# Performance work log

Measured on AMD Instinct MI355X. Metric: run time of the kernel, lower is better.

Reference implementation:

```python
import jax, jax.numpy as jnp
import numpy as np

EMB = 1024
HID = 2048
HEADS = 16
CONV = 4


def causal_conv1d(z, w):
    # z: [B, H, T], w: [H, K] depthwise causal conv
    K = w.shape[1]
    T = z.shape[-1]
    zp = jnp.pad(z, ((0, 0), (0, 0), (K - 1, 0)))  # [B, H, T+K-1]
    out = jnp.zeros_like(z)
    for k in range(K):  # tiny fixed loop over taps (K<=4)
        out = out + w[None, :, k, None] * jax.lax.dynamic_slice_in_dim(zp, k, T, axis=2)
    return out


def linear_scan(a, b):
    # h_t = a_t * h_{t-1} + b_t along last axis; associative scan
    def combine(c1, c2):
        a1, b1 = c1
        a2, b2 = c2
        return a1 * a2, a2 * b1 + b2
    _, h = jax.lax.associative_scan(combine, (a, b), axis=-1)
    return h


def setup_inputs() -> dict:
    key = jax.random.key(0)
    k1, k2, k3, k4 = jax.random.split(key, 4)
    x = jax.random.normal(k1, (4, 2048, EMB), dtype=jnp.float32)
    w1 = jax.random.normal(k2, (3 * HID, EMB), dtype=jnp.float32) * (EMB ** -0.5)
    w2 = jax.random.normal(k3, (EMB, HID), dtype=jnp.float32) * (HID ** -0.5)
    conv_weight = jax.random.normal(k4, (HID, CONV), dtype=jnp.float32) * (CONV ** -0.5)
    return {"x": x, "w1": w1, "w2": w2, "conv_weight": conv_weight}


def reference(x, w1, w2, conv_weight):
    bsz, seq_len, _ = x.shape
    head_dim = HID // HEADS
    y = jnp.einsum("bse,he->bsh", x, w1)  # [B, S, 3*HID]
    out1, z, h = jnp.split(y, 3, axis=-1)
    z = jnp.swapaxes(z, 1, 2)  # [B, HID, S]
    h = jnp.swapaxes(h, 1, 2)
    z = causal_conv1d(z, conv_weight)
    z = jax.nn.sigmoid(z)
    z = z.reshape(bsz * HEADS, head_dim, seq_len)
    h = h.reshape(bsz * HEADS, head_dim, seq_len)
    h = linear_scan(1.0 - z, z * h)
    out2 = jnp.swapaxes(h.reshape(bsz, HID, seq_len), 1, 2)  # [B, S, HID]
    out = jax.nn.silu(out1) * out2
    return jnp.einsum("bsh,eh->bse", out, w2)
```

## Files before the change

### kernel.cpp

```cpp
#include <hip/hip_runtime.h>
#include <cstdint>

#define EMB 1024
#define HID 2048
#define BATCH 4
#define SEQ 2048
#define MROWS (BATCH * SEQ)
#define N1 (3 * HID)
#define K1 EMB
#define N2 EMB
#define K2 HID

#define NX (MROWS * EMB)
#define NW1 (N1 * K1)
#define NW2 (N2 * K2)

#define SEG 32
#define SLEN (SEQ / SEG)

typedef unsigned short ushort_t;
typedef __bf16 bf16x8 __attribute__((ext_vector_type(8)));
typedef float f32x4 __attribute__((ext_vector_type(4)));
typedef ushort_t us4 __attribute__((ext_vector_type(4)));

__device__ __forceinline__ ushort_t f2bf(float f) {
    uint32_t u = __builtin_bit_cast(uint32_t, f);
    u += 0x7fffu + ((u >> 16) & 1u);
    return (ushort_t)(u >> 16);
}
__device__ __forceinline__ float bf2f(ushort_t h) {
    uint32_t u = ((uint32_t)h) << 16;
    return __builtin_bit_cast(float, u);
}
__device__ __forceinline__ float bflo(uint32_t v) {
    return __builtin_bit_cast(float, v << 16);
}
__device__ __forceinline__ float bfhi(uint32_t v) {
    return __builtin_bit_cast(float, v & 0xffff0000u);
}
__device__ __forceinline__ float sigm(float x) {
    return 1.f / (1.f + __expf(-x));
}

__device__ __forceinline__ void gload_lds16(const ushort_t* g, const ushort_t* l) {
    __builtin_amdgcn_global_load_lds(
        (const __attribute__((address_space(1))) void*)(uintptr_t)(g),
        (__attribute__((address_space(3))) void*)(uint32_t)(uintptr_t)(l),
        16, 0, 0);
}

__global__ __launch_bounds__(256) void cvt_kernel(
    const float* __restrict__ x, const float* __restrict__ w1,
    const float* __restrict__ w2, ushort_t* __restrict__ xb,
    ushort_t* __restrict__ w1b, ushort_t* __restrict__ w2b) {
    const int i = (blockIdx.x * 256 + threadIdx.x) * 4;
    const float* s;
    ushort_t* d;
    if (i < NX) {
        s = x + i; d = xb + i;
    } else if (i < NX + NW1) {
        s = w1 + (i - NX); d = w1b + (i - NX);
    } else {
        s = w2 + (i - NX - NW1); d = w2b + (i - NX - NW1);
    }
    const float4 v = *(const float4*)s;
    us4 o;
    o.x = f2bf(v.x); o.y = f2bf(v.y); o.z = f2bf(v.z); o.w = f2bf(v.w);
    *(us4*)d = o;
}

template <bool OUT_BF16>
__global__ __launch_bounds__(256) void gemm_bt(
    const ushort_t* __restrict__ A, const ushort_t* __restrict__ B,
    void* __restrict__ Cv, int M, int N, int K) {
    __shared__ ushort_t sA[2 * 128 * 32];
    __shared__ ushort_t sB[2 * 128 * 32];

    const int tid  = threadIdx.x;
    const int lane = tid & 63;
    const int wave = tid >> 6;
    const int quad = lane >> 4;
    const int l16  = lane & 15;
    const long tm0 = (long)blockIdx.y * 128;
    const long tn0 = (long)blockIdx.x * 128;
    const int wm = (wave & 1) * 64;
    const int wn = (wave >> 1) * 64;

    f32x4 acc[4][4] = {};

    const int ar0 = tid >> 2;
    const int ar1 = (tid + 256) >> 2;
    const int kq  = (tid & 3) ^ ((ar0 >> 1) & 3);
    const int ac  = kq * 8;
    const ushort_t* gA = A + (size_t)tm0 * K;
    const ushort_t* gB = B + (size_t)tn0 * K;

    const int rsw = (l16 >> 1) & 3;
    const int aoff = (quad ^ rsw) * 8 + l16 * 32;

    for (int k0 = 0; k0 < K; k0 += 64) {
        __syncthreads();
#pragma unroll
        for (int p = 0; p < 2; ++p) {
            const int kp = k0 + p * 32;
            ushort_t* pA = &sA[p * 4096];
            ushort_t* pB = &sB[p * 4096];
            gload_lds16(gA + (size_t)ar0 * K + kp + ac, pA + wave * 512);
            gload_lds16(gA + (size_t)ar1 * K + kp + ac, pA + 2048 + wave * 512);
            gload_lds16(gB + (size_t)ar0 * K + kp + ac, pB + wave * 512);
            gload_lds16(gB + (size_t)ar1 * K + kp + ac, pB + 2048 + wave * 512);
        }
        __syncthreads();

#pragma unroll
        for (int p = 0; p < 2; ++p) {
            const ushort_t* pA = &sA[p * 4096];
            const ushort_t* pB = &sB[p * 4096];
            bf16x8 af[4], bfr[4];
#pragma unroll
            for (int i = 0; i < 4; ++i)
                af[i] = *(const bf16x8*)&pA[(wm + i * 16) * 32 + aoff];
#pragma unroll
            for (int j = 0; j < 4; ++j)
                bfr[j] = *(const bf16x8*)&pB[(wn + j * 16) * 32 + aoff];
#pragma unroll
            for (int i = 0; i < 4; ++i)
#pragma unroll
                for (int j = 0; j < 4; ++j)
                    acc[i][j] = __builtin_amdgcn_mfma_f32_16x16x32_bf16(
                        af[i], bfr[j], acc[i][j], 0, 0, 0);
        }
    }

#pragma unroll
    for (int i = 0; i < 4; ++i) {
        const long row0 = tm0 + wm + i * 16 + quad * 4;
#pragma unroll
        for (int j = 0; j < 4; ++j) {
            const long col = tn0 + wn + j * 16 + l16;
#pragma unroll
            for (int r = 0; r < 4; ++r) {
                if constexpr (OUT_BF16) {
                    ((ushort_t*)Cv)[(size_t)(row0 + r) * N + col] = f2bf(acc[i][j][r]);
                } else {
                    ((float*)Cv)[(size_t)(row0 + r) * N + col] = acc[i][j][r];
                }
            }
        }
    }
}

__device__ __forceinline__ void lda4(bf16x8 (&af)[2][4], const ushort_t* c,
                                     int arow, int quad, int sw) {
#pragma unroll
    for (int s = 0; s < 2; ++s)
#pragma unroll
        for (int i = 0; i < 4; ++i)
            af[s][i] = *(const bf16x8*)&c[(arow + i * 16) * 64 +
                                          (((s * 4 + quad) ^ sw) << 3)];
}
__device__ __forceinline__ void ldb2(bf16x8 (&bfr)[2][2], const ushort_t* c,
                                     int bcol, int quad, int sw) {
#pragma unroll
    for (int s = 0; s < 2; ++s)
#pragma unroll
        for (int j = 0; j < 2; ++j)
            bfr[s][j] = *(const bf16x8*)&c[(bcol + j * 16) * 64 +
                                           (((s * 4 + quad) ^ sw) << 3)];
}
template <int QM, int QN>
__device__ __forceinline__ void mm16(f32x4 (&acc)[8][4],
                                     const bf16x8 (&af)[2][4],
                                     const bf16x8 (&bfr)[2][2]) {
#pragma unroll
    for (int s = 0; s < 2; ++s)
#pragma unroll
        for (int i = 0; i < 4; ++i)
#pragma unroll
            for (int j = 0; j < 2; ++j)
                acc[QM * 4 + i][QN * 2 + j] =
                    __builtin_amdgcn_mfma_f32_16x16x32_bf16(
                        af[s][i], bfr[s][j], acc[QM * 4 + i][QN * 2 + j], 0, 0, 0);
}

template <bool OUT_BF16>
__global__ __launch_bounds__(512, 2) void gemm256(
    const ushort_t* __restrict__ A, const ushort_t* __restrict__ B,
    void* __restrict__ Cv, int M, int N, int K) {
    __shared__ __align__(16) ushort_t sA[2][2][8192];
    __shared__ __align__(16) ushort_t sB[2][2][8192];

    const int tid  = threadIdx.x;
    const int lane = tid & 63;
    const int wave = tid >> 6;
    const int wm   = wave >> 2;
    const int wn   = wave & 3;
    const int quad = lane >> 4;
    const int l15  = lane & 15;
    const int sw   = lane & 7;

    int wg = blockIdx.x;
    const int nwg = gridDim.x;
    if ((nwg & 7) == 0) wg = (wg & 7) * (nwg >> 3) + (wg >> 3);
    const int nbx = N >> 8;
    const int bx = wg % nbx;
    const int by = wg / nbx;
    const long tm0 = (long)by << 8;
    const long tn0 = (long)bx << 8;

    const ushort_t* gA = A + (size_t)tm0 * K;
    const ushort_t* gB = B + (size_t)tn0 * K;

    const int l8 = lane >> 3;
    const int ss = (lane & 7) ^ l8;
    const uint32_t rA = (uint32_t)((wave & 3) * 16 + l8 + (wave >> 2) * 128);
    const int cB = wave * 16 + l8;
    const uint32_t rB = (uint32_t)((cB >> 5) * 64 + (cB & 31));
    const uint32_t offA0 = rA * (uint32_t)K + (uint32_t)ss * 8u;
    const uint32_t offA1 = offA0 + 8u * (uint32_t)K;
    const uint32_t offB0 = rB * (uint32_t)K + (uint32_t)ss * 8u;
    const uint32_t offB1 = offB0 + 8u * (uint32_t)K;

    const auto stA = [&](int tt, int q) {
        ushort_t* d = &sA[tt & 1][q][wave << 10];
        const size_t ko = (size_t)tt * 64 + (size_t)q * 64 * (size_t)K;
        gload_lds16(gA + ko + offA0, d);
        gload_lds16(gA + ko + offA1, d + 512);
    };
    const auto stB = [&](int tt, int q) {
        ushort_t* d = &sB[tt & 1][q][wave << 10];
        const size_t ko = (size_t)tt * 64 + (size_t)q * 32 * (size_t)K;
        gload_lds16(gB + ko + offB0, d);
        gload_lds16(gB + ko + offB1, d + 512);
    };

    const int arow = wm * 64 + l15;
    const int bcol = wn * 32 + l15;

    f32x4 acc[8][4] = {};
    bf16x8 af[2][4], bfr[2][2];

    const int NT = K >> 6;

    stA(0, 0); stB(0, 0); stB(0, 1); stA(0, 1);
    stA(1, 0); stB(1, 1); stA(1, 1);
    asm volatile("s_waitcnt vmcnt(6)" ::: "memory");
    __builtin_amdgcn_s_barrier();

    for (int T = 0; T < NT; ++T) {
        const int cur = T & 1;
        const ushort_t* a0 = &sA[cur][0][0];
        const ushort_t* a1 = &sA[cur][1][0];
        const ushort_t* b0 = &sB[cur][0][0];
        const ushort_t* b1 = &sB[cur][1][0];
        const bool st1 = (T + 1 < NT);
        const bool st2 = (T + 2 < NT);

        lda4(af, a0, arow, quad, sw);
        ldb2(bfr, b0, bcol, quad, sw);
        if (st1) stB(T + 1, 0);
        asm volatile("s_waitcnt lgkmcnt(8)" ::: "memory");
        __builtin_amdgcn_s_barrier();
        asm volatile("s_waitcnt lgkmcnt(0)" ::: "memory");
        __builtin_amdgcn_s_setprio(1);
        mm16<0, 0>(acc, af, bfr);
        __builtin_amdgcn_s_setprio(0);
        __builtin_amdgcn_s_barrier();

        ldb2(bfr, b1, bcol, quad, sw);
        if (st2) stA(T + 2, 0);
        __builtin_amdgcn_s_barrier();
        asm volatile("s_waitcnt lgkmcnt(0)" ::: "memory");
        __builtin_amdgcn_s_setprio(1);
        mm16<0, 1>(acc, af, bfr);
        __builtin_amdgcn_s_setprio(0);
        __builtin_amdgcn_s_barrier();

        lda4(af, a1, arow, quad, sw);
        if (st2) stB(T + 2, 1);
        __builtin_amdgcn_s_barrier();
        asm volatile("s_waitcnt lgkmcnt(0)" ::: "memory");
        __builtin_amdgcn_s_setprio(1);
        mm16<1, 1>(acc, af, bfr);
        __builtin_amdgcn_s_setprio(0);
        __builtin_amdgcn_s_barrier();

        ldb2(bfr, b0, bcol, quad, sw);
        if (st2) stA(T + 2, 1);
        __builtin_amdgcn_s_barrier();
        asm volatile("s_waitcnt lgkmcnt(0)" ::: "memory");
        __builtin_amdgcn_s_setprio(1);
        mm16<1, 0>(acc, af, bfr);
        __builtin_amdgcn_s_setprio(0);
        if (st2)      asm volatile("s_waitcnt vmcnt(6)" ::: "memory");
        else if (st1) asm volatile("s_waitcnt vmcnt(0)" ::: "memory");
        __builtin_amdgcn_s_barrier();
    }

#pragma unroll
    for (int ai = 0; ai < 8; ++ai) {
        const long row0 = tm0 + wm * 128 + (ai >> 2) * 64 + (ai & 3) * 16 + quad * 4;
#pragma unroll
        for (int bj = 0; bj < 4; ++bj) {
            const long col = tn0 + wn * 64 + (bj >> 1) * 32 + (bj & 1) * 16 + l15;
#pragma unroll
            for (int r = 0; r < 4; ++r) {
                if constexpr (OUT_BF16) {
                    ((ushort_t*)Cv)[(size_t)(row0 + r) * N + col] = f2bf(acc[ai][bj][r]);
                } else {
                    ((float*)Cv)[(size_t)(row0 + r) * N + col] = acc[ai][bj][r];
                }
            }
        }
    }
}

__global__ __launch_bounds__(256) void scan_part1(
    const ushort_t* __restrict__ y, const float* __restrict__ cw,
    float* __restrict__ Ag, float* __restrict__ Bg) {
    const int gid = blockIdx.x * 256 + threadIdx.x;
    const int ch  = (gid & 1023) * 2;
    const int bs  = gid >> 10;
    const int b   = bs >> 5;
    const int seg = bs & 31;
    const int t0  = seg * SLEN;
    const size_t rowbase = (size_t)b * SEQ;
    const ushort_t* yz = y + 2048 + ch;
    const ushort_t* yh = y + 4096 + ch;

    float w[2][4];
#pragma unroll
    for (int c = 0; c < 2; ++c)
#pragma unroll
        for (int k = 0; k < 4; ++k) w[c][k] = cw[(ch + c) * 4 + k];

    auto ld2 = [&](const ushort_t* p, int t) -> uint32_t {
        return *(const uint32_t*)(p + (rowbase + (size_t)t) * 6144);
    };
    auto zpair = [&](int t, float* out) {
        if (t < 0) { out[0] = 0.f; out[1] = 0.f; }
        else { uint32_t v = ld2(yz, t); out[0] = bflo(v); out[1] = bfhi(v); }
    };

    float z1[2], z2[2], z3[2], A[2] = {1.f, 1.f}, Bv[2] = {0.f, 0.f};
    zpair(t0 - 1, z1); zpair(t0 - 2, z2); zpair(t0 - 3, z3);

#pragma unroll 4
    for (int t = t0; t < t0 + SLEN; ++t) {
        const uint32_t vz = ld2(yz, t);
        const uint32_t vh = ld2(yh, t);
        const float zr[2] = {bflo(vz), bfhi(vz)};
        const float hr[2] = {bflo(vh), bfhi(vh)};
#pragma unroll
        for (int c = 0; c < 2; ++c) {
            const float cv = w[c][0] * z3[c] + w[c][1] * z2[c] +
                             w[c][2] * z1[c] + w[c][3] * zr[c];
            const float s = sigm(cv);
            z3[c] = z2[c]; z2[c] = z1[c]; z1[c] = zr[c];
            const float a = 1.f - s;
            A[c] *= a;
            Bv[c] = a * Bv[c] + s * hr[c];
        }
    }
    const size_t idx = ((size_t)b * SEG + seg) * HID + ch;
    *(float2*)&Ag[idx] = make_float2(A[0], A[1]);
    *(float2*)&Bg[idx] = make_float2(Bv[0], Bv[1]);
}

__global__ __launch_bounds__(256) void scan_part2(
    const float* __restrict__ Ag, const float* __restrict__ Bg,
    float* __restrict__ Cr) {
    const int gid = blockIdx.x * 256 + threadIdx.x;
    const int b  = gid >> 11;
    const int ch = gid & 2047;
    float carry = 0.f;
#pragma unroll
    for (int s = 0; s < SEG; ++s) {
        const size_t idx = ((size_t)b * SEG + s) * HID + ch;
        Cr[idx] = carry;
        carry = Ag[idx] * carry + Bg[idx];
    }
}

__global__ __launch_bounds__(256) void scan_part3(
    const ushort_t* __restrict__ y, const float* __restrict__ cw,
    const float* __restrict__ Cr, ushort_t* __restrict__ u) {
    const int gid = blockIdx.x * 256 + threadIdx.x;
    const int ch  = (gid & 1023) * 2;
    const int bs  = gid >> 10;
    const int b   = bs >> 5;
    const int seg = bs & 31;
    const int t0  = seg * SLEN;
    const size_t rowbase = (size_t)b * SEQ;
    const ushort_t* yo = y + ch;
    const ushort_t* yz = y + 2048 + ch;
    const ushort_t* yh = y + 4096 + ch;

    float w[2][4];
#pragma unroll
    for (int c = 0; c < 2; ++c)
#pragma unroll
        for (int k = 0; k < 4; ++k) w[c][k] = cw[(ch + c) * 4 + k];

    auto ld2 = [&](const ushort_t* p, int t) -> uint32_t {
        return *(const uint32_t*)(p + (rowbase + (size_t)t) * 6144);
    };
    auto zpair = [&](int t, float* out) {
        if (t < 0) { out[0] = 0.f; out[1] = 0.f; }
        else { uint32_t v = ld2(yz, t); out[0] = bflo(v); out[1] = bfhi(v); }
    };

    const size_t cidx = ((size_t)b * SEG + seg) * HID + ch;
    float h[2] = {Cr[cidx], Cr[cidx + 1]};
    float z1[2], z2[2], z3[2];
    zpair(t0 - 1, z1); zpair(t0 - 2, z2); zpair(t0 - 3, z3);

#pragma unroll 4
    for (int t = t0; t < t0 + SLEN; ++t) {
        const uint32_t vz = ld2(yz, t);
        const uint32_t vh = ld2(yh, t);
        const uint32_t vo = ld2(yo, t);
        const float zr[2] = {bflo(vz), bfhi(vz)};
        const float hr[2] = {bflo(vh), bfhi(vh)};
        const float o1[2] = {bflo(vo), bfhi(vo)};
        ushort_t res[2];
#pragma unroll
        for (int c = 0; c < 2; ++c) {
            const float cv = w[c][0] * z3[c] + w[c][1] * z2[c] +
                             w[c][2] * z1[c] + w[c][3] * zr[c];
            const float s = sigm(cv);
            z3[c] = z2[c]; z2[c] = z1[c]; z1[c] = zr[c];
            h[c] = (1.f - s) * h[c] + s * hr[c];
            const float sil = o1[c] * sigm(o1[c]);
            res[c] = f2bf(sil * h[c]);
        }
        *(uint32_t*)&u[(rowbase + (size_t)t) * (size_t)HID + ch] =
            (uint32_t)res[0] | ((uint32_t)res[1] << 16);
    }
}

extern "C" void kernel_launch(void* const* d_in, const int* in_sizes, int n_in,
                              void* d_out, int out_size, void* d_ws, size_t ws_size,
                              hipStream_t stream) {
    const float* x  = (const float*)d_in[0];
    const float* w1 = (const float*)d_in[1];
    const float* w2 = (const float*)d_in[2];
    const float* cw = (const float*)d_in[3];
    char* ws = (char*)d_ws;

    ushort_t* xb  = (ushort_t*)(ws);
    ushort_t* w1b = (ushort_t*)(ws + (size_t)16777216);
    ushort_t* w2b = (ushort_t*)(ws + (size_t)29360128);
    ushort_t* y   = (ushort_t*)(ws + (size_t)33554432);
    ushort_t* u   = (ushort_t*)(ws + (size_t)134217728);
    float* Ag = (float*)(ws);
    float* Bg = (float*)(ws + (size_t)1048576);
    float* Cr = (float*)(ws + (size_t)2097152);
    float* out = (float*)d_out;

    cvt_kernel<<<16384, 256, 0, stream>>>(x, w1, w2, xb, w1b, w2b);
    gemm256<true><<<dim3(768), 512, 0, stream>>>(xb, w1b, (void*)y, MROWS, N1, K1);
    scan_part1<<<512, 256, 0, stream>>>(y, cw, Ag, Bg);
    scan_part2<<<32, 256, 0, stream>>>(Ag, Bg, Cr);
    scan_part3<<<512, 256, 0, stream>>>(y, cw, Cr, u);
    gemm_bt<false><<<dim3(N2 / 128, MROWS / 128), 256, 0, stream>>>(
        u, w2b, (void*)out, MROWS, N2, K2);
}
```

Before: 325.4 us.

## Load all LDS fragments upfront per K-tile and cut barriers in GEMM loop

The GEMM main loop now reads both A halves and both B halves from LDS into separate register sets at the start of each K-tile, instead of reloading fragments before each of the four MFMA quadrants. This lets the loop drop most per-quadrant barriers and lgkmcnt waits, so the global-to-LDS stores are regrouped into three phases instead of four. The cost is roughly double the fragment registers, which may lower occupancy. Removing the barriers that separated the fragment reads from the next LDS overwrites also risks write-after-read hazards on the double-buffered tiles.

```diff
diff --git a/kernel.cpp b/kernel.cpp
--- a/kernel.cpp
+++ b/kernel.cpp
@@ -238,7 +238,7 @@
     const int bcol = wn * 32 + l15;
 
     f32x4 acc[8][4] = {};
-    bf16x8 af[2][4], bfr[2][2];
+    bf16x8 af0[2][4], af1[2][4], bf0[2][2], bf1[2][2];
 
     const int NT = K >> 6;
 
@@ -256,41 +256,26 @@
         const bool st1 = (T + 1 < NT);
         const bool st2 = (T + 2 < NT);
 
-        lda4(af, a0, arow, quad, sw);
-        ldb2(bfr, b0, bcol, quad, sw);
+        lda4(af0, a0, arow, quad, sw);
+        ldb2(bf0, b0, bcol, quad, sw);
+        ldb2(bf1, b1, bcol, quad, sw);
+        lda4(af1, a1, arow, quad, sw);
         if (st1) stB(T + 1, 0);
-        asm volatile("s_waitcnt lgkmcnt(8)" ::: "memory");
-        __builtin_amdgcn_s_barrier();
-        asm volatile("s_waitcnt lgkmcnt(0)" ::: "memory");
         __builtin_amdgcn_s_setprio(1);
-        mm16<0, 0>(acc, af, bfr);
+        mm16<0, 0>(acc, af0, bf0);
         __builtin_amdgcn_s_setprio(0);
         __builtin_amdgcn_s_barrier();
 
-        ldb2(bfr, b1, bcol, quad, sw);
         if (st2) stA(T + 2, 0);
-        __builtin_amdgcn_s_barrier();
-        asm volatile("s_waitcnt lgkmcnt(0)" ::: "memory");
         __builtin_amdgcn_s_setprio(1);
-        mm16<0, 1>(acc, af, bfr);
+        mm16<0, 1>(acc, af0, bf1);
+        mm16<1, 0>(acc, af1, bf0);
         __builtin_amdgcn_s_setprio(0);
         __builtin_amdgcn_s_barrier();
 
-        lda4(af, a1, arow, quad, sw);
-        if (st2) stB(T + 2, 1);
-        __builtin_amdgcn_s_barrier();
-        asm volatile("s_waitcnt lgkmcnt(0)" ::: "memory");
+        if (st2) { stB(T + 2, 1); stA(T + 2, 1); }
         __builtin_amdgcn_s_setprio(1);
-        mm16<1, 1>(acc, af, bfr);
-        __builtin_amdgcn_s_setprio(0);
-        __builtin_amdgcn_s_barrier();
-
-        ldb2(bfr, b0, bcol, quad, sw);
-        if (st2) stA(T + 2, 1);
-        __builtin_amdgcn_s_barrier();
-        asm volatile("s_waitcnt lgkmcnt(0)" ::: "memory");
-        __builtin_amdgcn_s_setprio(1);
-        mm16<1, 0>(acc, af, bfr);
+        mm16<1, 1>(acc, af1, bf1);
         __builtin_amdgcn_s_setprio(0);
         if (st2)      asm volatile("s_waitcnt vmcnt(6)" ::: "memory");
         else if (st1) asm volatile("s_waitcnt vmcnt(0)" ::: "memory");
```

New measurement: 316.3 us. -2.8%, faster.
